# Performance work log

Hardware: AMD Instinct MI355X
Metric: run time of the kernel (lower is better)

Reference implementation:

```python
import jax, jax.numpy as jnp
import numpy as np

FIELD_DIMS = (339, 5825, 64)
RANK = 128
NUM_CHANNELS = 256
BATCH = 131072
NUM_MODES = len(FIELD_DIMS)


def setup_inputs() -> dict:
    key = jax.random.key(0)
    ks = jax.random.split(key, 12)
    # per-mode in-range indices, shape (B, num_modes)
    cols = [jax.random.randint(ks[i], (BATCH,), 0, FIELD_DIMS[i]) for i in range(NUM_MODES)]
    indices = jnp.stack(cols, axis=1).astype(jnp.int64)
    # embedding tables (one per tensor mode)
    emb0 = jax.random.normal(ks[3], (FIELD_DIMS[0], RANK), jnp.float32) * 0.1
    emb1 = jax.random.normal(ks[4], (FIELD_DIMS[1], RANK), jnp.float32) * 0.1
    emb2 = jax.random.normal(ks[5], (FIELD_DIMS[2], RANK), jnp.float32) * 0.1
    # conv1: Conv2d(1, C, kernel=(rank,1)) -> weight (C, rank) after squeeze
    w1 = jax.random.normal(ks[6], (NUM_CHANNELS, RANK), jnp.float32) * (1.0 / np.sqrt(RANK))
    b1 = jnp.zeros((NUM_CHANNELS,), jnp.float32)
    # conv2: Conv2d(C, C, kernel=(1,num_modes)) -> weight (C_out, C_in, num_modes)
    w2 = jax.random.normal(ks[7], (NUM_CHANNELS, NUM_CHANNELS, NUM_MODES), jnp.float32) * (1.0 / np.sqrt(NUM_CHANNELS * NUM_MODES))
    b2 = jnp.zeros((NUM_CHANNELS,), jnp.float32)
    # aggregation MLP
    wfc1 = jax.random.normal(ks[8], (NUM_CHANNELS, NUM_CHANNELS), jnp.float32) * (1.0 / np.sqrt(NUM_CHANNELS))
    bfc1 = jnp.zeros((NUM_CHANNELS,), jnp.float32)
    wfc2 = jax.random.normal(ks[9], (1, NUM_CHANNELS), jnp.float32) * (1.0 / np.sqrt(NUM_CHANNELS))
    bfc2 = jnp.zeros((1,), jnp.float32)
    return {"indices": indices, "emb0": emb0, "emb1": emb1, "emb2": emb2,
            "w1": w1, "b1": b1, "w2": w2, "b2": b2,
            "wfc1": wfc1, "bfc1": bfc1, "wfc2": wfc2, "bfc2": bfc2}


def reference(indices, emb0, emb1, emb2, w1, b1, w2, b2, wfc1, bfc1, wfc2, bfc2):
    # EmbeddingModule: (B, rank, num_modes)
    x = jnp.stack([emb0[indices[:, 0]], emb1[indices[:, 1]], emb2[indices[:, 2]]], axis=2)
    # conv1 over rank dim (kernel (rank,1)): (B, C, num_modes)
    h = jax.nn.relu(jnp.einsum('brm,cr->bcm', x, w1) + b1[None, :, None])
    # conv2 over mode dim (kernel (1,num_modes)): (B, C)
    h = jax.nn.relu(jnp.einsum('bcm,dcm->bd', h, w2) + b2)
    # AggregationModule MLP
    h = jax.nn.relu(h @ wfc1.T + bfc1)
    out = jax.nn.relu(h @ wfc2.T + bfc2)  # (B, 1)
    return out.squeeze(-1)  # (B,)
```

## Files before the change

kernel.cpp:

```cpp
#include <hip/hip_runtime.h>

typedef __bf16 bf16;
typedef __bf16 bf16x4 __attribute__((ext_vector_type(4)));
typedef __bf16 bf16x8 __attribute__((ext_vector_type(8)));
typedef float  f32x4  __attribute__((ext_vector_type(4)));
typedef unsigned int uint32;

#define BT 64

#define N_E0 (339*128)
#define N_E1 (5825*128)
#define N_E2 (64*128)
#define N_W1 (256*128)
#define N_W2 (256*768)
#define N_F1 (256*256)
#define N_F2 256
#define O_E0 0
#define O_E1 (O_E0+N_E0)
#define O_E2 (O_E1+N_E1)
#define O_W1 (O_E2+N_E2)
#define O_W2 (O_W1+N_W1)
#define O_F1 (O_W2+N_W2)
#define O_F2 (O_F1+N_F1)
#define N_TOT (O_F2+N_F2)

#define BYTES_BF16 ((size_t)N_TOT*2)
#define OFF_FLOAT  BYTES_BF16
#define OFF_FLAG   (OFF_FLOAT + 772*4)
#define OFF_IDX    (OFF_FLAG + 16)
#define N_IDX      (131072*3)
#define OFF_Q      (OFF_IDX + (size_t)N_IDX*4)

#define QB0 0
#define QB1 (339*256)
#define QB2 (QB1 + 5825*256)

static __device__ __forceinline__ f32x4 mfma16(bf16x8 a, bf16x8 b, f32x4 c) {
    return __builtin_amdgcn_mfma_f32_16x16x32_bf16(a, b, c, 0, 0, 0);
}

__global__ __launch_bounds__(256)
void convert_all(const void* __restrict__ e0, const void* __restrict__ e1,
                 const void* __restrict__ e2, const void* __restrict__ w1r,
                 const void* __restrict__ b1r, const void* __restrict__ w2r,
                 const void* __restrict__ b2r, const void* __restrict__ f1r,
                 const void* __restrict__ fc1br, const void* __restrict__ f2r,
                 const void* __restrict__ fc2br, const void* __restrict__ idxr,
                 bf16* __restrict__ wsb, float* __restrict__ wsf,
                 int* __restrict__ flagp, int* __restrict__ idx32)
{
    __shared__ int sF;
    const int tid = threadIdx.x;
    const int bid = blockIdx.x;
    if (tid == 0) sF = 0;
    __syncthreads();

    if (bid < 256) {
        if (((const uint32*)idxr)[tid * 2 + 1] != 0) atomicOr(&sF, 1);
        __syncthreads();
        const bool i64 = (sF == 0);
        #pragma unroll
        for (int it = 0; it < 6; ++it) {
            int k = bid * 1536 + it * 256 + tid;
            if (k < N_IDX) {
                long long v = i64 ? ((const long long*)idxr)[k]
                                  : (long long)((const int*)idxr)[k];
                int m = k - (k / 3) * 3;
                long long dim = (m == 0 ? 339 : (m == 1 ? 5825 : 64));
                v = v < 0 ? 0 : (v >= dim ? dim - 1 : v);
                idx32[k] = (int)v;
            }
        }
        return;
    }

    if (tid < 64) {
        uint32 e = (((const uint32*)w1r)[tid] >> 7) & 0xffu;
        if (e > 126u) atomicOr(&sF, 1);
    }
    __syncthreads();
    const bool fp32 = (sF != 0);

    if (bid < 768) {
        const unsigned n4 = (O_W2 + (N_TOT - O_F1)) / 4;
        for (unsigned u = (bid - 256) * 256u + tid; u < n4; u += 512u * 256u) {
            unsigned e = u * 4, dst = e;
            const void* src; unsigned off;
            if (e < O_W2) {
                if (e < O_E1)      { src = e0;  off = e; }
                else if (e < O_E2) { src = e1;  off = e - O_E1; }
                else if (e < O_W1) { src = e2;  off = e - O_E2; }
                else               { src = w1r; off = e - O_W1; }
            } else {
                dst = O_F1 + (e - O_W2);
                if (dst < O_F2) {
                    src = f1r; off = dst - O_F1;
                    unsigned ee = off >> 8, kk = off & 255u;
                    dst = O_F1 + ((((ee >> 4) * 8u + (kk >> 5)) * 64u
                                   + ((kk >> 3) & 3u) * 16u + (ee & 15u)) << 3) + (kk & 7u);
                } else { src = f2r; off = dst - O_F2; }
            }
            if (fp32) {
                float4 v = *(const float4*)((const float*)src + off);
                bf16x4 o; o[0]=(bf16)v.x; o[1]=(bf16)v.y; o[2]=(bf16)v.z; o[3]=(bf16)v.w;
                *(bf16x4*)(wsb + dst) = o;
            } else {
                *(uint2*)(wsb + dst) = *(const uint2*)((const bf16*)src + off);
            }
        }
    } else if (bid < 1008) {
        for (unsigned i = (bid - 768) * 256u + tid; i < (unsigned)N_W2; i += 240u * 256u) {
            unsigned d = i / 768u, r = i - d * 768u;
            unsigned m = r >> 8, c = r & 255u;
            unsigned off = d * 768u + c * 3u + m;
            wsb[O_W2 + i] = fp32 ? (bf16)((const float*)w2r)[off] : ((const bf16*)w2r)[off];
        }
    } else {
        if (tid == 0) *flagp = fp32 ? 1 : 0;
        #pragma unroll
        for (int it = 0; it < 4; ++it) {
            int j = it * 256 + tid;
            if (j < 769) {
                const void* src; int off;
                if (j < 256)      { src = b1r;   off = j; }
                else if (j < 512) { src = b2r;   off = j - 256; }
                else if (j < 768) { src = fc1br; off = j - 512; }
                else              { src = fc2br; off = 0; }
                wsf[j] = fp32 ? ((const float*)src)[off] : (float)((const bf16*)src)[off];
            }
        }
    }
}

__global__ __launch_bounds__(256, 2)
void build_q(const bf16* __restrict__ wsb, const float* __restrict__ wsf,
             bf16* __restrict__ Qt)
{
    __shared__ alignas(16) bf16 sX[64 * 136];
    __shared__ alignas(16) bf16 sPE[64 * 264];

    const int tid  = threadIdx.x;
    const int wave = tid >> 6;
    const int lane = tid & 63;
    const int quad = lane >> 4;
    const int l15  = lane & 15;
    const int bid  = blockIdx.x;

    int m, row0, dim, embBase, qBase;
    if (bid < 6)       { m = 0; row0 = bid * 64;        dim = 339;  embBase = O_E0; qBase = QB0; }
    else if (bid < 98) { m = 1; row0 = (bid - 6) * 64;  dim = 5825; embBase = O_E1; qBase = QB1; }
    else               { m = 2; row0 = 0;               dim = 64;   embBase = O_E2; qBase = QB2; }

    const bf16* w1  = wsb + O_W1;
    const bf16* w2t = wsb + O_W2;
    const float* fb1 = wsf;

    {
        int row = tid >> 2, seg = tid & 3;
        int r = row0 + row; r = r >= dim ? dim - 1 : r;
        const uint4* s4 = (const uint4*)(wsb + embBase + (size_t)r * 128 + seg * 32);
        uint4* d4 = (uint4*)(&sX[row * 136 + seg * 32]);
        #pragma unroll
        for (int u = 0; u < 4; ++u) d4[u] = s4[u];
    }
    __syncthreads();

    const f32x4 zero4 = {0.f, 0.f, 0.f, 0.f};

    #pragma unroll
    for (int mtl = 0; mtl < 4; ++mtl) {
        int mt = wave * 4 + mtl;
        int c  = mt * 16 + l15;
        bf16x8 aw[4];
        #pragma unroll
        for (int ks = 0; ks < 4; ++ks)
            aw[ks] = *(const bf16x8*)(w1 + c * 128 + ks * 32 + quad * 8);
        const float4 bv = *(const float4*)(fb1 + mt * 16 + quad * 4);
        #pragma unroll
        for (int nt = 0; nt < 4; ++nt) {
            f32x4 acc = zero4;
            #pragma unroll
            for (int ks = 0; ks < 4; ++ks) {
                bf16x8 xb = *(const bf16x8*)(&sX[(nt * 16 + l15) * 136 + ks * 32 + quad * 8]);
                acc = mfma16(aw[ks], xb, acc);
            }
            bf16x4 hv;
            hv[0] = (bf16)fmaxf(acc[0] + bv.x, 0.f);
            hv[1] = (bf16)fmaxf(acc[1] + bv.y, 0.f);
            hv[2] = (bf16)fmaxf(acc[2] + bv.z, 0.f);
            hv[3] = (bf16)fmaxf(acc[3] + bv.w, 0.f);
            *(bf16x4*)(&sPE[(nt * 16 + l15) * 264 + mt * 16 + quad * 4]) = hv;
        }
    }
    __syncthreads();

    f32x4 acc2[4][4];
    #pragma unroll
    for (int i = 0; i < 4; ++i)
        #pragma unroll
        for (int j = 0; j < 4; ++j) acc2[i][j] = zero4;
    #pragma unroll
    for (int ks = 0; ks < 8; ++ks) {
        bf16x8 af[4], bfr[4];
        #pragma unroll
        for (int mt = 0; mt < 4; ++mt)
            af[mt] = *(const bf16x8*)(&sPE[(mt * 16 + l15) * 264 + ks * 32 + quad * 8]);
        #pragma unroll
        for (int nt = 0; nt < 4; ++nt) {
            int d = wave * 64 + nt * 16 + l15;
            bfr[nt] = *(const bf16x8*)(w2t + d * 768 + m * 256 + ks * 32 + quad * 8);
        }
        #pragma unroll
        for (int mt = 0; mt < 4; ++mt)
            #pragma unroll
            for (int nt = 0; nt < 4; ++nt)
                acc2[mt][nt] = mfma16(af[mt], bfr[nt], acc2[mt][nt]);
    }
    #pragma unroll
    for (int nt = 0; nt < 4; ++nt) {
        int d = wave * 64 + nt * 16 + l15;
        #pragma unroll
        for (int mt = 0; mt < 4; ++mt)
            #pragma unroll
            for (int r = 0; r < 4; ++r) {
                int rl = mt * 16 + quad * 4 + r;
                if (row0 + rl < dim)
                    Qt[qBase + (size_t)(row0 + rl) * 256 + d] = (bf16)acc2[mt][nt][r];
            }
    }
}

__global__ __launch_bounds__(256, 4)
void costco_main(const bf16* __restrict__ wsb, const bf16* __restrict__ Qt,
                 const float* __restrict__ wsf, const int* __restrict__ flagp,
                 const int* __restrict__ idx32, void* __restrict__ out)
{
    __shared__ alignas(16) bf16 sH2[BT * 264];
    __shared__ float sRed[BT];
    __shared__ int sIdx[BT * 3];

    const bf16* wf   = wsb + O_F1;
    const bf16* wfc2 = wsb + O_F2;
    const float* fb2  = wsf + 256;
    const float* fbc1 = wsf + 512;
    const float  bfc2v = wsf[768];
    const int fp32out = *flagp;

    const int tid  = threadIdx.x;
    const int wave = tid >> 6;
    const int lane = tid & 63;
    const int quad = lane >> 4;
    const int l15  = lane & 15;
    const int bbase = blockIdx.x * BT;

    if (tid < BT * 3) sIdx[tid] = idx32[bbase * 3 + tid];
    if (tid < BT) sRed[tid] = bfc2v;
    __syncthreads();

    {
        const int half = lane >> 5;
        const int l31  = lane & 31;
        float bb[8];
        {
            float4 t0 = *(const float4*)(fb2 + l31 * 8);
            float4 t1 = *(const float4*)(fb2 + l31 * 8 + 4);
            bb[0]=t0.x; bb[1]=t0.y; bb[2]=t0.z; bb[3]=t0.w;
            bb[4]=t1.x; bb[5]=t1.y; bb[6]=t1.z; bb[7]=t1.w;
        }
        #pragma unroll
        for (int rp = 0; rp < 8; ++rp) {
            const int r  = wave * 16 + rp * 2 + half;
            const int i0 = sIdx[r * 3 + 0];
            const int i1 = sIdx[r * 3 + 1];
            const int i2 = sIdx[r * 3 + 2];
            bf16x8 a = *(const bf16x8*)(Qt + QB0 + (size_t)i0 * 256 + l31 * 8);
            bf16x8 b = *(const bf16x8*)(Qt + QB1 + (size_t)i1 * 256 + l31 * 8);
            bf16x8 c = *(const bf16x8*)(Qt + QB2 + (size_t)i2 * 256 + l31 * 8);
            bf16x8 o;
            #pragma unroll
            for (int j = 0; j < 8; ++j) {
                float v = (float)a[j] + (float)b[j] + (float)c[j] + bb[j];
                o[j] = (bf16)fmaxf(v, 0.f);
            }
            *(bf16x8*)(&sH2[r * 264 + l31 * 8]) = o;
        }
    }
    __syncthreads();

    const f32x4 zero4 = {0.f, 0.f, 0.f, 0.f};

    f32x4 acc3[4][4];
    #pragma unroll
    for (int i = 0; i < 4; ++i)
        #pragma unroll
        for (int j = 0; j < 4; ++j) acc3[i][j] = zero4;
    #pragma unroll
    for (int ks = 0; ks < 8; ++ks) {
        bf16x8 af[4], bfr[4];
        #pragma unroll
        for (int mt = 0; mt < 4; ++mt)
            af[mt] = *(const bf16x8*)(&sH2[(mt * 16 + l15) * 264 + ks * 32 + quad * 8]);
        #pragma unroll
        for (int nt = 0; nt < 4; ++nt)
            bfr[nt] = *(const bf16x8*)(wf + ((size_t)((wave * 4 + nt) * 8 + ks) * 64 + lane) * 8);
        #pragma unroll
        for (int mt = 0; mt < 4; ++mt)
            #pragma unroll
            for (int nt = 0; nt < 4; ++nt)
                acc3[mt][nt] = mfma16(af[mt], bfr[nt], acc3[mt][nt]);
    }

    float wv[4], bc[4];
    #pragma unroll
    for (int nt = 0; nt < 4; ++nt) {
        int e = wave * 64 + nt * 16 + l15;
        wv[nt] = (float)wfc2[e];
        bc[nt] = fbc1[e];
    }
    #pragma unroll
    for (int mt = 0; mt < 4; ++mt)
        #pragma unroll
        for (int r = 0; r < 4; ++r) {
            float p = 0.f;
            #pragma unroll
            for (int nt = 0; nt < 4; ++nt)
                p += fmaxf(acc3[mt][nt][r] + bc[nt], 0.f) * wv[nt];
            p += __shfl_xor(p, 1, 64);
            p += __shfl_xor(p, 2, 64);
            p += __shfl_xor(p, 4, 64);
            p += __shfl_xor(p, 8, 64);
            if (l15 == 0) atomicAdd(&sRed[mt * 16 + quad * 4 + r], p);
        }
    __syncthreads();

    if (tid < BT) {
        float v = fmaxf(sRed[tid], 0.f);
        if (fp32out) ((float*)out)[bbase + tid] = v;
        else         ((bf16*)out)[bbase + tid] = (bf16)v;
    }
}

extern "C" void kernel_launch(void* const* d_in, const int* in_sizes, int n_in,
                              void* d_out, int out_size, void* d_ws, size_t ws_size,
                              hipStream_t stream) {
    char* ws = (char*)d_ws;
    bf16*  wsb   = (bf16*)ws;
    float* wsf   = (float*)(ws + OFF_FLOAT);
    int*   flagp = (int*)(ws + OFF_FLAG);
    int*   idx32 = (int*)(ws + OFF_IDX);
    bf16*  Qt    = (bf16*)(ws + OFF_Q);

    hipLaunchKernelGGL(convert_all, dim3(1009), dim3(256), 0, stream,
                       d_in[1], d_in[2], d_in[3], d_in[4], d_in[5], d_in[6],
                       d_in[7], d_in[8], d_in[9], d_in[10], d_in[11], d_in[0],
                       wsb, wsf, flagp, idx32);

    hipLaunchKernelGGL(build_q, dim3(99), dim3(256), 0, stream, wsb, wsf, Qt);

    const int B = 131072;
    hipLaunchKernelGGL(costco_main, dim3(B / BT), dim3(256), 0, stream,
                       wsb, Qt, wsf, flagp, idx32, d_out);
}
```

Before: 120.5 us.

## Pre-swizzle weights into MFMA fragment layout and shrink build_q tiles

The conversion kernel now writes embedding tables, conv1 weights, conv2 weights and fc1 weights directly in MFMA fragment order. This lets build_q load operands straight from global memory into registers without staging through shared memory. build_q now processes 16-row tiles, giving 391 blocks instead of 99, to spread the precompute across more CUs. The final reduction in the main kernel replaces shared-memory atomicAdd with per-wave partial sums that are added afterwards. The trade-off is more blocks and repeated global reads of the conv1/conv2 weights for each small tile.

```diff
diff --git a/kernel.cpp b/kernel.cpp
--- a/kernel.cpp
+++ b/kernel.cpp
@@ -8,21 +8,17 @@
 
 #define BT 64
 
-#define N_E0 (339*128)
-#define N_E1 (5825*128)
-#define N_E2 (64*128)
-#define N_W1 (256*128)
-#define N_W2 (256*768)
-#define N_F1 (256*256)
-#define N_F2 256
-#define O_E0 0
-#define O_E1 (O_E0+N_E0)
-#define O_E2 (O_E1+N_E1)
-#define O_W1 (O_E2+N_E2)
-#define O_W2 (O_W1+N_W1)
-#define O_F1 (O_W2+N_W2)
-#define O_F2 (O_F1+N_F1)
-#define N_TOT (O_F2+N_F2)
+#define N_EF0 (22*2048)
+#define N_EF1 (365*2048)
+#define N_EF2 (4*2048)
+#define O_EF0 0
+#define O_EF1 (O_EF0+N_EF0)
+#define O_EF2 (O_EF1+N_EF1)
+#define O_W1F (O_EF2+N_EF2)
+#define O_W2F (O_W1F+32768)
+#define O_F1  (O_W2F+196608)
+#define O_F2  (O_F1+65536)
+#define N_TOT (O_F2+256)
 
 #define BYTES_BF16 ((size_t)N_TOT*2)
 #define OFF_FLOAT  BYTES_BF16
@@ -37,6 +33,11 @@
 
 static __device__ __forceinline__ f32x4 mfma16(bf16x8 a, bf16x8 b, f32x4 c) {
     return __builtin_amdgcn_mfma_f32_16x16x32_bf16(a, b, c, 0, 0, 0);
+}
+
+static __device__ __forceinline__ unsigned frag_off(unsigned ee, unsigned kk, unsigned nks) {
+    return (((ee >> 4) * nks + (kk >> 5)) * 64u + ((kk >> 3) & 3u) * 16u + (ee & 15u)) * 8u
+           + (kk & 7u);
 }
 
 __global__ __launch_bounds__(256)
@@ -82,23 +83,22 @@
     const bool fp32 = (sF != 0);
 
     if (bid < 768) {
-        const unsigned n4 = (O_W2 + (N_TOT - O_F1)) / 4;
+        const unsigned n4 = 895744u / 4u;
         for (unsigned u = (bid - 256) * 256u + tid; u < n4; u += 512u * 256u) {
-            unsigned e = u * 4, dst = e;
-            const void* src; unsigned off;
-            if (e < O_W2) {
-                if (e < O_E1)      { src = e0;  off = e; }
-                else if (e < O_E2) { src = e1;  off = e - O_E1; }
-                else if (e < O_W1) { src = e2;  off = e - O_E2; }
-                else               { src = w1r; off = e - O_W1; }
+            unsigned e = u * 4;
+            const void* src; unsigned off, dst;
+            if (e < 829952u) {
+                unsigned base;
+                if (e < 43392u)       { src = e0;  off = e;           base = O_EF0; }
+                else if (e < 788992u) { src = e1;  off = e - 43392u;  base = O_EF1; }
+                else if (e < 797184u) { src = e2;  off = e - 788992u; base = O_EF2; }
+                else                  { src = w1r; off = e - 797184u; base = O_W1F; }
+                dst = base + frag_off(off >> 7, off & 127u, 4u);
+            } else if (e < 895488u) {
+                src = f1r; off = e - 829952u;
+                dst = O_F1 + frag_off(off >> 8, off & 255u, 8u);
             } else {
-                dst = O_F1 + (e - O_W2);
-                if (dst < O_F2) {
-                    src = f1r; off = dst - O_F1;
-                    unsigned ee = off >> 8, kk = off & 255u;
-                    dst = O_F1 + ((((ee >> 4) * 8u + (kk >> 5)) * 64u
-                                   + ((kk >> 3) & 3u) * 16u + (ee & 15u)) << 3) + (kk & 7u);
-                } else { src = f2r; off = dst - O_F2; }
+                src = f2r; off = e - 895488u; dst = O_F2 + off;
             }
             if (fp32) {
                 float4 v = *(const float4*)((const float*)src + off);
@@ -109,11 +109,13 @@
             }
         }
     } else if (bid < 1008) {
-        for (unsigned i = (bid - 768) * 256u + tid; i < (unsigned)N_W2; i += 240u * 256u) {
-            unsigned d = i / 768u, r = i - d * 768u;
-            unsigned m = r >> 8, c = r & 255u;
+        for (unsigned i = (bid - 768) * 256u + tid; i < 196608u; i += 240u * 256u) {
+            unsigned m = i >> 16, r = i & 65535u;
+            unsigned dt = r >> 12, ks = (r >> 9) & 7u, lane = (r >> 3) & 63u, j = r & 7u;
+            unsigned d = dt * 16u + (lane & 15u);
+            unsigned c = ks * 32u + (lane >> 4) * 8u + j;
             unsigned off = d * 768u + c * 3u + m;
-            wsb[O_W2 + i] = fp32 ? (bf16)((const float*)w2r)[off] : ((const bf16*)w2r)[off];
+            wsb[O_W2F + i] = fp32 ? (bf16)((const float*)w2r)[off] : ((const bf16*)w2r)[off];
         }
     } else {
         if (tid == 0) *flagp = fp32 ? 1 : 0;
@@ -132,12 +134,11 @@
     }
 }
 
-__global__ __launch_bounds__(256, 2)
+__global__ __launch_bounds__(256)
 void build_q(const bf16* __restrict__ wsb, const float* __restrict__ wsf,
              bf16* __restrict__ Qt)
 {
-    __shared__ alignas(16) bf16 sX[64 * 136];
-    __shared__ alignas(16) bf16 sPE[64 * 264];
+    __shared__ alignas(16) bf16 sPE[4096];
 
     const int tid  = threadIdx.x;
     const int wave = tid >> 6;
@@ -146,87 +147,65 @@
     const int l15  = lane & 15;
     const int bid  = blockIdx.x;
 
-    int m, row0, dim, embBase, qBase;
-    if (bid < 6)       { m = 0; row0 = bid * 64;        dim = 339;  embBase = O_E0; qBase = QB0; }
-    else if (bid < 98) { m = 1; row0 = (bid - 6) * 64;  dim = 5825; embBase = O_E1; qBase = QB1; }
-    else               { m = 2; row0 = 0;               dim = 64;   embBase = O_E2; qBase = QB2; }
-
-    const bf16* w1  = wsb + O_W1;
-    const bf16* w2t = wsb + O_W2;
+    int m, tile, dim, efBase, qBase;
+    if (bid < 22)       { m = 0; tile = bid;       dim = 339;  efBase = O_EF0; qBase = QB0; }
+    else if (bid < 387) { m = 1; tile = bid - 22;  dim = 5825; efBase = O_EF1; qBase = QB1; }
+    else                { m = 2; tile = bid - 387; dim = 64;   efBase = O_EF2; qBase = QB2; }
+    const int row0 = tile * 16;
+
+    const bf16* w1f = wsb + O_W1F;
+    const bf16* w2f = wsb + O_W2F + m * 65536;
     const float* fb1 = wsf;
-
-    {
-        int row = tid >> 2, seg = tid & 3;
-        int r = row0 + row; r = r >= dim ? dim - 1 : r;
-        const uint4* s4 = (const uint4*)(wsb + embBase + (size_t)r * 128 + seg * 32);
-        uint4* d4 = (uint4*)(&sX[row * 136 + seg * 32]);
-        #pragma unroll
-        for (int u = 0; u < 4; ++u) d4[u] = s4[u];
-    }
-    __syncthreads();
-
     const f32x4 zero4 = {0.f, 0.f, 0.f, 0.f};
+
+    bf16x8 be[4];
+    #pragma unroll
+    for (int ks = 0; ks < 4; ++ks)
+        be[ks] = *(const bf16x8*)(wsb + efBase + (size_t)((tile * 4 + ks) * 64 + lane) * 8);
 
     #pragma unroll
     for (int mtl = 0; mtl < 4; ++mtl) {
         int mt = wave * 4 + mtl;
-        int c  = mt * 16 + l15;
-        bf16x8 aw[4];
-        #pragma unroll
-        for (int ks = 0; ks < 4; ++ks)
-            aw[ks] = *(const bf16x8*)(w1 + c * 128 + ks * 32 + quad * 8);
+        f32x4 acc = zero4;
+        #pragma unroll
+        for (int ks = 0; ks < 4; ++ks) {
+            bf16x8 aw = *(const bf16x8*)(w1f + ((mt * 4 + ks) * 64 + lane) * 8);
+            acc = mfma16(aw, be[ks], acc);
+        }
         const float4 bv = *(const float4*)(fb1 + mt * 16 + quad * 4);
+        bf16x4 hv;
+        hv[0] = (bf16)fmaxf(acc[0] + bv.x, 0.f);
+        hv[1] = (bf16)fmaxf(acc[1] + bv.y, 0.f);
+        hv[2] = (bf16)fmaxf(acc[2] + bv.z, 0.f);
+        hv[3] = (bf16)fmaxf(acc[3] + bv.w, 0.f);
+        int ksq   = mt >> 1;
+        int quadq = ((mt & 1) << 1) | (quad >> 1);
+        int j0    = (quad & 1) * 4;
+        *(bf16x4*)(&sPE[(ksq * 64 + quadq * 16 + l15) * 8 + j0]) = hv;
+    }
+    __syncthreads();
+
+    f32x4 acc2[4];
+    #pragma unroll
+    for (int nt = 0; nt < 4; ++nt) acc2[nt] = zero4;
+    #pragma unroll
+    for (int ks = 0; ks < 8; ++ks) {
+        bf16x8 af = *(const bf16x8*)(&sPE[(ks * 64 + lane) * 8]);
         #pragma unroll
         for (int nt = 0; nt < 4; ++nt) {
-            f32x4 acc = zero4;
-            #pragma unroll
-            for (int ks = 0; ks < 4; ++ks) {
-                bf16x8 xb = *(const bf16x8*)(&sX[(nt * 16 + l15) * 136 + ks * 32 + quad * 8]);
-                acc = mfma16(aw[ks], xb, acc);
-            }
-            bf16x4 hv;
-            hv[0] = (bf16)fmaxf(acc[0] + bv.x, 0.f);
-            hv[1] = (bf16)fmaxf(acc[1] + bv.y, 0.f);
-            hv[2] = (bf16)fmaxf(acc[2] + bv.z, 0.f);
-            hv[3] = (bf16)fmaxf(acc[3] + bv.w, 0.f);
-            *(bf16x4*)(&sPE[(nt * 16 + l15) * 264 + mt * 16 + quad * 4]) = hv;
-        }
-    }
-    __syncthreads();
-
-    f32x4 acc2[4][4];
-    #pragma unroll
-    for (int i = 0; i < 4; ++i)
-        #pragma unroll
-        for (int j = 0; j < 4; ++j) acc2[i][j] = zero4;
-    #pragma unroll
-    for (int ks = 0; ks < 8; ++ks) {
-        bf16x8 af[4], bfr[4];
-        #pragma unroll
-        for (int mt = 0; mt < 4; ++mt)
-            af[mt] = *(const bf16x8*)(&sPE[(mt * 16 + l15) * 264 + ks * 32 + quad * 8]);
-        #pragma unroll
-        for (int nt = 0; nt < 4; ++nt) {
-            int d = wave * 64 + nt * 16 + l15;
-            bfr[nt] = *(const bf16x8*)(w2t + d * 768 + m * 256 + ks * 32 + quad * 8);
-        }
-        #pragma unroll
-        for (int mt = 0; mt < 4; ++mt)
-            #pragma unroll
-            for (int nt = 0; nt < 4; ++nt)
-                acc2[mt][nt] = mfma16(af[mt], bfr[nt], acc2[mt][nt]);
+            bf16x8 bw = *(const bf16x8*)(w2f + (size_t)(((wave * 4 + nt) * 8 + ks) * 64 + lane) * 8);
+            acc2[nt] = mfma16(af, bw, acc2[nt]);
+        }
     }
     #pragma unroll
     for (int nt = 0; nt < 4; ++nt) {
-        int d = wave * 64 + nt * 16 + l15;
-        #pragma unroll
-        for (int mt = 0; mt < 4; ++mt)
-            #pragma unroll
-            for (int r = 0; r < 4; ++r) {
-                int rl = mt * 16 + quad * 4 + r;
-                if (row0 + rl < dim)
-                    Qt[qBase + (size_t)(row0 + rl) * 256 + d] = (bf16)acc2[mt][nt][r];
-            }
+        int d = (wave * 4 + nt) * 16 + l15;
+        #pragma unroll
+        for (int r = 0; r < 4; ++r) {
+            int rl = quad * 4 + r;
+            if (row0 + rl < dim)
+                Qt[qBase + (size_t)(row0 + rl) * 256 + d] = (bf16)acc2[nt][r];
+        }
     }
 }
 
@@ -236,7 +215,7 @@
                  const int* __restrict__ idx32, void* __restrict__ out)
 {
     __shared__ alignas(16) bf16 sH2[BT * 264];
-    __shared__ float sRed[BT];
+    __shared__ float sPart[4][BT];
     __shared__ int sIdx[BT * 3];
 
     const bf16* wf   = wsb + O_F1;
@@ -254,7 +233,6 @@
     const int bbase = blockIdx.x * BT;
 
     if (tid < BT * 3) sIdx[tid] = idx32[bbase * 3 + tid];
-    if (tid < BT) sRed[tid] = bfc2v;
     __syncthreads();
 
     {
@@ -329,12 +307,13 @@
             p += __shfl_xor(p, 2, 64);
             p += __shfl_xor(p, 4, 64);
             p += __shfl_xor(p, 8, 64);
-            if (l15 == 0) atomicAdd(&sRed[mt * 16 + quad * 4 + r], p);
+            if (l15 == 0) sPart[wave][mt * 16 + quad * 4 + r] = p;
         }
     __syncthreads();
 
     if (tid < BT) {
-        float v = fmaxf(sRed[tid], 0.f);
+        float v = sPart[0][tid] + sPart[1][tid] + sPart[2][tid] + sPart[3][tid] + bfc2v;
+        v = fmaxf(v, 0.f);
         if (fp32out) ((float*)out)[bbase + tid] = v;
         else         ((bf16*)out)[bbase + tid] = (bf16)v;
     }
@@ -355,7 +334,7 @@
                        d_in[7], d_in[8], d_in[9], d_in[10], d_in[11], d_in[0],
                        wsb, wsf, flagp, idx32);
 
-    hipLaunchKernelGGL(build_q, dim3(99), dim3(256), 0, stream, wsb, wsf, Qt);
+    hipLaunchKernelGGL(build_q, dim3(391), dim3(256), 0, stream, wsb, wsf, Qt);
 
     const int B = 131072;
     hipLaunchKernelGGL(costco_main, dim3(B / BT), dim3(256), 0, stream,
```

New measurement: 117.8 us. 1.02x faster.
